# Kernel optimization log

Hardware: AMD Instinct MI355X
Metric: run time of the kernel (lower is better)

Reference implementation:

```python
import jax, jax.numpy as jnp
import numpy as np

GRID_SIZE = 5
SPLINE_ORDER = 3
GRID_RANGE = (-1.0, 1.0)
IN_FEATURES = 1024
OUT_FEATURES = 1024
N_TOKENS = 8192
N_BASIS = GRID_SIZE + SPLINE_ORDER  # number of B-spline basis functions per input feature


def make_grid(dtype=jnp.float32):
    # Extended knot vector: grid_size+1 interior knots over grid_range, padded by
    # spline_order knots on each side (efficient-KAN convention; the intended
    # semantics of the TF port's b_splines recursion).
    h = (GRID_RANGE[1] - GRID_RANGE[0]) / GRID_SIZE
    idx = jnp.arange(-SPLINE_ORDER, GRID_SIZE + SPLINE_ORDER + 1, dtype=dtype)
    return idx * h + GRID_RANGE[0]  # [grid_size + 2*spline_order + 1]


def b_splines(x, grid):
    # x: [N, in] -> bases: [N, in, N_BASIS] via de Boor / Cox recursion.
    x3 = x[..., None]  # [N, in, 1]
    g = grid  # [K], broadcasts against last axis
    bases = ((x3 >= g[:-1]) & (x3 < g[1:])).astype(x.dtype)  # order-0: [N, in, K-1]
    for k in range(1, SPLINE_ORDER + 1):
        left = (x3 - g[: -(k + 1)]) / (g[k:-1] - g[: -(k + 1)])
        right = (g[k + 1:] - x3) / (g[k + 1:] - g[1:-k])
        bases = left * bases[..., :-1] + right * bases[..., 1:]
    return bases  # [N, in, N_BASIS]


def setup_inputs() -> dict:
    key = jax.random.key(0)
    k1, k2, k3, k4 = jax.random.split(key, 4)
    x = jax.random.uniform(k1, (N_TOKENS, IN_FEATURES), dtype=jnp.float32)
    base_weight = jax.random.normal(k2, (IN_FEATURES, OUT_FEATURES), dtype=jnp.float32) * 0.02
    spline_weight = jax.random.normal(k3, (OUT_FEATURES, IN_FEATURES, N_BASIS), dtype=jnp.float32) * 0.02
    spline_scaler = jax.random.normal(k4, (OUT_FEATURES, IN_FEATURES), dtype=jnp.float32) * 0.1
    return {"x": x, "base_weight": base_weight, "spline_weight": spline_weight,
            "spline_scaler": spline_scaler}


def reference(x, base_weight, spline_weight, spline_scaler):
    grid = make_grid(x.dtype)
    # base path: silu(x) @ W_base
    base_out = jnp.matmul(jax.nn.silu(x), base_weight)  # [N, out]
    # spline path: grouped contraction over (in_feature, basis)
    bases = b_splines(x, grid)  # [N, in, nb]
    sw = spline_weight * spline_scaler[..., None]  # standalone scale: [out, in, nb]
    spline_out = jnp.einsum('nib,oib->no', bases, sw)
    return base_out + spline_out  # [N, out]
```

## Files before the change

kernel.cpp:

```cpp
#include <hip/hip_runtime.h>
#include <hip/hip_bf16.h>
#include <stdint.h>

typedef unsigned short u16;
typedef __attribute__((ext_vector_type(8))) __bf16 bf16x8;
typedef __attribute__((ext_vector_type(4))) float f32x4;

#define NTOK 8192
#define NIN  1024
#define NOUT 1024
#define KTOT 9216
#define BM 128
#define BN 256
#define BK 64
#define NT (KTOT / BK)
#define ABUF (BM * BK)
#define BBUF (BN * BK)
#define TBUF (ABUF + BBUF)

#define PB_BLOCKS 1024
#define PS_BLOCKS 4096
#define BA_BLOCKS 32768

__device__ __forceinline__ u16 f2bf(float f) {
  union { float f; unsigned u; } v; v.f = f;
  unsigned r = v.u + 0x7FFFu + ((v.u >> 16) & 1u);
  return (u16)(r >> 16);
}

__device__ __forceinline__ void gload_lds16(const void* g, void* l) {
  __builtin_amdgcn_global_load_lds(
      (__attribute__((address_space(1))) void*)(uintptr_t)g,
      (__attribute__((address_space(3))) void*)(uintptr_t)l, 16, 0, 0);
}

__global__ void prep_all(const float* __restrict__ X, const float* __restrict__ W,
                         const float* __restrict__ SW, const float* __restrict__ SS,
                         u16* __restrict__ Bt, u16* __restrict__ A) {
  __shared__ float tile[32][33];
  const int b = blockIdx.x;
  const int tid = threadIdx.x;

  if (b < PB_BLOCKS) {
    int i0 = (b & 31) * 32, o0 = (b >> 5) * 32;
    int tx = tid & 31, ty = tid >> 5;
#pragma unroll
    for (int r = 0; r < 4; ++r)
      tile[ty + 8 * r][tx] = W[(size_t)(i0 + ty + 8 * r) * NOUT + o0 + tx];
    __syncthreads();
#pragma unroll
    for (int r = 0; r < 4; ++r)
      Bt[(size_t)(o0 + ty + 8 * r) * KTOT + i0 + tx] = f2bf(tile[tx][ty + 8 * r]);
  } else if (b < PB_BLOCKS + PS_BLOCKS) {
    int idx = (b - PB_BLOCKS) * 256 + tid;
    int o = idx >> 10, i = idx & 1023;
    float s = SS[idx];
    const float4* p = (const float4*)(SW + (size_t)idx * 8);
    float4 a = p[0], c = p[1];
    union { u16 us[8]; uint4 v; } pk;
    pk.us[0] = f2bf(a.x * s); pk.us[1] = f2bf(a.y * s);
    pk.us[2] = f2bf(a.z * s); pk.us[3] = f2bf(a.w * s);
    pk.us[4] = f2bf(c.x * s); pk.us[5] = f2bf(c.y * s);
    pk.us[6] = f2bf(c.z * s); pk.us[7] = f2bf(c.w * s);
    *(uint4*)(Bt + (size_t)o * KTOT + NIN + (size_t)i * 8) = pk.v;
  } else {
    int idx = (b - PB_BLOCKS - PS_BLOCKS) * 256 + tid;
    int n = idx >> 10, i = idx & 1023;
    float x = X[idx];
    float sx = x / (1.f + __expf(-x));
    A[(size_t)n * KTOT + i] = f2bf(sx);
    float bb[11];
#pragma unroll
    for (int j = 0; j < 11; ++j) {
      float gj  = 0.4f * j - 2.2f;
      float gj1 = 0.4f * (j + 1) - 2.2f;
      bb[j] = (x >= gj && x < gj1) ? 1.f : 0.f;
    }
#pragma unroll
    for (int k = 1; k <= 3; ++k) {
      float inv = 1.f / (0.4f * k);
#pragma unroll
      for (int j = 0; j + k < 11; ++j) {
        float gj = 0.4f * j - 2.2f;
        float left  = (x - gj) * inv;
        float right = (0.4f * (j + k + 1) - 2.2f - x) * inv;
        bb[j] = left * bb[j] + right * bb[j + 1];
      }
    }
    union { u16 us[8]; uint4 v; } pk;
#pragma unroll
    for (int j = 0; j < 8; ++j) pk.us[j] = f2bf(bb[j]);
    *(uint4*)(A + (size_t)n * KTOT + NIN + (size_t)i * 8) = pk.v;
  }
}


__global__ __launch_bounds__(512, 2) void kan_gemm(const u16* __restrict__ A,
                                                   const u16* __restrict__ Bt,
                                                   float* __restrict__ C) {
  __shared__ u16 lds[3 * TBUF];
  const int tid = threadIdx.x;
  const int w = tid >> 6, l = tid & 63;
  const int wr = w >> 2, wc = w & 3;
  const int l4 = l >> 4, lc = l & 15;

  const int bid = blockIdx.x;
  const int xcd = bid & 7, jj = bid >> 3;
  const int bn = xcd >> 1;
  const int bm = (xcd & 1) * 32 + jj;

  const u16* Ab = A  + (size_t)bm * BM * KTOT;
  const u16* Bb = Bt + (size_t)bn * BN * KTOT;

  int srcA[2], dstA[2], srcB[4], dstB[4];
#pragma unroll
  for (int it = 0; it < 2; ++it) {
    int c = it * 512 + tid, r = c >> 3, s = (c & 7) ^ (r & 7);
    srcA[it] = r * KTOT + s * 8;
    dstA[it] = (it * 512 + w * 64) * 8;
  }
#pragma unroll
  for (int it = 0; it < 4; ++it) {
    int c = it * 512 + tid, r = c >> 3, s = (c & 7) ^ (r & 7);
    srcB[it] = r * KTOT + s * 8;
    dstB[it] = ABUF + (it * 512 + w * 64) * 8;
  }

  int rA[4], rB[4];
#pragma unroll
  for (int m = 0; m < 4; ++m) rA[m] = wr * 64 + m * 16 + lc;
#pragma unroll
  for (int n = 0; n < 4; ++n) rB[n] = wc * 64 + n * 16 + lc;

  f32x4 acc[4][4];
#pragma unroll
  for (int m = 0; m < 4; ++m)
#pragma unroll
    for (int n = 0; n < 4; ++n)
      acc[m][n] = f32x4{0.f, 0.f, 0.f, 0.f};

#pragma unroll
  for (int it = 0; it < 2; ++it) gload_lds16(Ab + srcA[it], &lds[dstA[it]]);
#pragma unroll
  for (int it = 0; it < 4; ++it) gload_lds16(Bb + srcB[it], &lds[dstB[it]]);
#pragma unroll
  for (int it = 0; it < 2; ++it) gload_lds16(Ab + srcA[it] + BK, &lds[TBUF + dstA[it]]);
#pragma unroll
  for (int it = 0; it < 4; ++it) gload_lds16(Bb + srcB[it] + BK, &lds[TBUF + dstB[it]]);
  asm volatile("s_waitcnt vmcnt(6)" ::: "memory");
  __builtin_amdgcn_s_barrier();

  int cur = 0;
  for (int t = 0; t < NT; ++t) {
    const int curo = cur * TBUF;
    const int nxto = ((cur == 0) ? 2 : cur - 1) * TBUF;
    const bool pf = (t + 2) < NT;
    const int k0n = (t + 2) * BK;

    if (pf) {
#pragma unroll
      for (int it = 0; it < 2; ++it) gload_lds16(Ab + srcA[it] + k0n, &lds[nxto + dstA[it]]);
#pragma unroll
      for (int it = 0; it < 4; ++it) gload_lds16(Bb + srcB[it] + k0n, &lds[nxto + dstB[it]]);
    }

    bf16x8 a_frag[4][2], b_frag[4][2];
#pragma unroll
    for (int m = 0; m < 4; ++m)
#pragma unroll
      for (int kk = 0; kk < 2; ++kk)
        a_frag[m][kk] = *(const bf16x8*)&lds[curo + rA[m] * 64 + (((kk * 4 + l4) ^ (rA[m] & 7)) * 8)];
#pragma unroll
    for (int n = 0; n < 4; ++n)
#pragma unroll
      for (int kk = 0; kk < 2; ++kk)
        b_frag[n][kk] = *(const bf16x8*)&lds[curo + ABUF + rB[n] * 64 + (((kk * 4 + l4) ^ (rB[n] & 7)) * 8)];

    asm volatile("s_waitcnt lgkmcnt(0)" ::: "memory");
    __builtin_amdgcn_sched_barrier(0);
    __builtin_amdgcn_s_setprio(1);
#pragma unroll
    for (int kk = 0; kk < 2; ++kk)
#pragma unroll
      for (int m = 0; m < 4; ++m)
#pragma unroll
        for (int n = 0; n < 4; ++n)
          acc[m][n] = __builtin_amdgcn_mfma_f32_16x16x32_bf16(a_frag[m][kk], b_frag[n][kk], acc[m][n], 0, 0, 0);
    __builtin_amdgcn_s_setprio(0);

    if (t >= NT - 2) { asm volatile("s_waitcnt vmcnt(0)" ::: "memory"); }
    else             { asm volatile("s_waitcnt vmcnt(6)" ::: "memory"); }
    __builtin_amdgcn_s_barrier();

    cur = (cur == 2) ? 0 : cur + 1;
  }

  const int row0 = bm * BM + wr * 64 + l4 * 4;
  const int col0 = bn * BN + wc * 64 + lc;
#pragma unroll
  for (int m = 0; m < 4; ++m)
#pragma unroll
    for (int n = 0; n < 4; ++n) {
      float* cp = C + (size_t)(row0 + m * 16) * NOUT + col0 + n * 16;
#pragma unroll
      for (int r = 0; r < 4; ++r)
        cp[(size_t)r * NOUT] = acc[m][n][r];
    }
}

extern "C" void kernel_launch(void* const* d_in, const int* in_sizes, int n_in,
                              void* d_out, int out_size, void* d_ws, size_t ws_size,
                              hipStream_t stream) {
  const float* x  = (const float*)d_in[0];
  const float* bw = (const float*)d_in[1];
  const float* sw = (const float*)d_in[2];
  const float* ss = (const float*)d_in[3];
  float* out = (float*)d_out;

  u16* Bt = (u16*)d_ws;
  u16* A  = (u16*)((char*)d_ws + (size_t)NOUT * KTOT * 2);

  prep_all<<<PB_BLOCKS + PS_BLOCKS + BA_BLOCKS, 256, 0, stream>>>(x, bw, sw, ss, Bt, A);
  kan_gemm<<<256, 512, 0, stream>>>(A, Bt, out);
}
```

Measured before the change: 281.3 us.

## Load A fragments directly from global into registers, bypassing LDS

The A operand is now fetched by each wave straight from global memory into registers, double-buffered one K-step ahead, and is no longer staged through LDS. Only the B tile goes through the triple-buffered LDS pipeline, which shrinks shared memory and removes the A LDS writes and reads. Waves that share rows of A now fetch the same data redundantly from global/L2. The vmcnt waits are retuned for the mixed register and LDS loads, and the loop is manually unrolled by two to alternate the A register buffers.

```diff
diff --git a/kernel.cpp b/kernel.cpp
--- a/kernel.cpp
+++ b/kernel.cpp
@@ -14,9 +14,7 @@
 #define BN 256
 #define BK 64
 #define NT (KTOT / BK)
-#define ABUF (BM * BK)
 #define BBUF (BN * BK)
-#define TBUF (ABUF + BBUF)
 
 #define PB_BLOCKS 1024
 #define PS_BLOCKS 4096
@@ -98,7 +96,7 @@
 __global__ __launch_bounds__(512, 2) void kan_gemm(const u16* __restrict__ A,
                                                    const u16* __restrict__ Bt,
                                                    float* __restrict__ C) {
-  __shared__ u16 lds[3 * TBUF];
+  __shared__ u16 lds[3 * BBUF];
   const int tid = threadIdx.x;
   const int w = tid >> 6, l = tid & 63;
   const int wr = w >> 2, wc = w & 3;
@@ -109,26 +107,19 @@
   const int bn = xcd >> 1;
   const int bm = (xcd & 1) * 32 + jj;
 
-  const u16* Ab = A  + (size_t)bm * BM * KTOT;
   const u16* Bb = Bt + (size_t)bn * BN * KTOT;
-
-  int srcA[2], dstA[2], srcB[4], dstB[4];
-#pragma unroll
-  for (int it = 0; it < 2; ++it) {
-    int c = it * 512 + tid, r = c >> 3, s = (c & 7) ^ (r & 7);
-    srcA[it] = r * KTOT + s * 8;
-    dstA[it] = (it * 512 + w * 64) * 8;
-  }
+  const u16* aBase = A + (size_t)(bm * 128 + wr * 64 + lc) * KTOT + l4 * 8;
+#define MSTRIDE ((size_t)16 * KTOT)
+
+  int srcB[4], dstB[4];
 #pragma unroll
   for (int it = 0; it < 4; ++it) {
     int c = it * 512 + tid, r = c >> 3, s = (c & 7) ^ (r & 7);
     srcB[it] = r * KTOT + s * 8;
-    dstB[it] = ABUF + (it * 512 + w * 64) * 8;
+    dstB[it] = (it * 512 + w * 64) * 8;
   }
 
-  int rA[4], rB[4];
-#pragma unroll
-  for (int m = 0; m < 4; ++m) rA[m] = wr * 64 + m * 16 + lc;
+  int rB[4];
 #pragma unroll
   for (int n = 0; n < 4; ++n) rB[n] = wc * 64 + n * 16 + lc;
 
@@ -139,60 +130,103 @@
     for (int n = 0; n < 4; ++n)
       acc[m][n] = f32x4{0.f, 0.f, 0.f, 0.f};
 
-#pragma unroll
-  for (int it = 0; it < 2; ++it) gload_lds16(Ab + srcA[it], &lds[dstA[it]]);
+  bf16x8 pA0[4][2], pA1[4][2];
+
+#pragma unroll
+  for (int m = 0; m < 4; ++m)
+#pragma unroll
+    for (int kk = 0; kk < 2; ++kk)
+      pA0[m][kk] = *(const bf16x8*)(aBase + m * MSTRIDE + kk * 32);
 #pragma unroll
   for (int it = 0; it < 4; ++it) gload_lds16(Bb + srcB[it], &lds[dstB[it]]);
 #pragma unroll
-  for (int it = 0; it < 2; ++it) gload_lds16(Ab + srcA[it] + BK, &lds[TBUF + dstA[it]]);
-#pragma unroll
-  for (int it = 0; it < 4; ++it) gload_lds16(Bb + srcB[it] + BK, &lds[TBUF + dstB[it]]);
-  asm volatile("s_waitcnt vmcnt(6)" ::: "memory");
+  for (int it = 0; it < 4; ++it) gload_lds16(Bb + srcB[it] + BK, &lds[BBUF + dstB[it]]);
+  asm volatile("s_waitcnt vmcnt(4)" ::: "memory");
   __builtin_amdgcn_s_barrier();
 
   int cur = 0;
-  for (int t = 0; t < NT; ++t) {
-    const int curo = cur * TBUF;
-    const int nxto = ((cur == 0) ? 2 : cur - 1) * TBUF;
-    const bool pf = (t + 2) < NT;
-    const int k0n = (t + 2) * BK;
-
-    if (pf) {
-#pragma unroll
-      for (int it = 0; it < 2; ++it) gload_lds16(Ab + srcA[it] + k0n, &lds[nxto + dstA[it]]);
-#pragma unroll
-      for (int it = 0; it < 4; ++it) gload_lds16(Bb + srcB[it] + k0n, &lds[nxto + dstB[it]]);
-    }
-
-    bf16x8 a_frag[4][2], b_frag[4][2];
-#pragma unroll
-    for (int m = 0; m < 4; ++m)
+#pragma unroll 1
+  for (int tp = 0; tp < NT / 2; ++tp) {
+    {
+      const int t = 2 * tp;
+      const int curo = cur * BBUF;
+      const int nxto = ((cur == 0) ? 2 : cur - 1) * BBUF;
+      const u16* aT1 = aBase + (size_t)(t + 1) * BK;
+
+#pragma unroll
+      for (int m = 0; m < 4; ++m)
+#pragma unroll
+        for (int kk = 0; kk < 2; ++kk)
+          pA1[m][kk] = *(const bf16x8*)(aT1 + m * MSTRIDE + kk * 32);
+      if (t + 2 < NT) {
+        const int k0n = (t + 2) * BK;
+#pragma unroll
+        for (int it = 0; it < 4; ++it) gload_lds16(Bb + srcB[it] + k0n, &lds[nxto + dstB[it]]);
+      }
+      __builtin_amdgcn_sched_barrier(0);
+      bf16x8 b_frag[4][2];
+#pragma unroll
+      for (int n = 0; n < 4; ++n)
+#pragma unroll
+        for (int kk = 0; kk < 2; ++kk)
+          b_frag[n][kk] = *(const bf16x8*)&lds[curo + rB[n] * 64 + (((kk * 4 + l4) ^ (rB[n] & 7)) * 8)];
+      asm volatile("s_waitcnt lgkmcnt(0)" ::: "memory");
+      __builtin_amdgcn_sched_barrier(0);
+      __builtin_amdgcn_s_setprio(1);
 #pragma unroll
       for (int kk = 0; kk < 2; ++kk)
-        a_frag[m][kk] = *(const bf16x8*)&lds[curo + rA[m] * 64 + (((kk * 4 + l4) ^ (rA[m] & 7)) * 8)];
-#pragma unroll
-    for (int n = 0; n < 4; ++n)
+#pragma unroll
+        for (int m = 0; m < 4; ++m)
+#pragma unroll
+          for (int n = 0; n < 4; ++n)
+            acc[m][n] = __builtin_amdgcn_mfma_f32_16x16x32_bf16(pA0[m][kk], b_frag[n][kk], acc[m][n], 0, 0, 0);
+      __builtin_amdgcn_s_setprio(0);
+      if (t == NT - 2) { asm volatile("s_waitcnt vmcnt(8)" ::: "memory"); }
+      else             { asm volatile("s_waitcnt vmcnt(12)" ::: "memory"); }
+      __builtin_amdgcn_s_barrier();
+      cur = (cur == 2) ? 0 : cur + 1;
+    }
+    {
+      const int t = 2 * tp + 1;
+      const int curo = cur * BBUF;
+      const int nxto = ((cur == 0) ? 2 : cur - 1) * BBUF;
+      const u16* aT1 = aBase + (size_t)(t + 1) * BK;
+
+      if (t + 1 < NT) {
+#pragma unroll
+        for (int m = 0; m < 4; ++m)
+#pragma unroll
+          for (int kk = 0; kk < 2; ++kk)
+            pA0[m][kk] = *(const bf16x8*)(aT1 + m * MSTRIDE + kk * 32);
+      }
+      if (t + 2 < NT) {
+        const int k0n = (t + 2) * BK;
+#pragma unroll
+        for (int it = 0; it < 4; ++it) gload_lds16(Bb + srcB[it] + k0n, &lds[nxto + dstB[it]]);
+      }
+      __builtin_amdgcn_sched_barrier(0);
+      bf16x8 b_frag[4][2];
+#pragma unroll
+      for (int n = 0; n < 4; ++n)
+#pragma unroll
+        for (int kk = 0; kk < 2; ++kk)
+          b_frag[n][kk] = *(const bf16x8*)&lds[curo + rB[n] * 64 + (((kk * 4 + l4) ^ (rB[n] & 7)) * 8)];
+      asm volatile("s_waitcnt lgkmcnt(0)" ::: "memory");
+      __builtin_amdgcn_sched_barrier(0);
+      __builtin_amdgcn_s_setprio(1);
 #pragma unroll
       for (int kk = 0; kk < 2; ++kk)
-        b_frag[n][kk] = *(const bf16x8*)&lds[curo + ABUF + rB[n] * 64 + (((kk * 4 + l4) ^ (rB[n] & 7)) * 8)];
-
-    asm volatile("s_waitcnt lgkmcnt(0)" ::: "memory");
-    __builtin_amdgcn_sched_barrier(0);
-    __builtin_amdgcn_s_setprio(1);
-#pragma unroll
-    for (int kk = 0; kk < 2; ++kk)
-#pragma unroll
-      for (int m = 0; m < 4; ++m)
-#pragma unroll
-        for (int n = 0; n < 4; ++n)
-          acc[m][n] = __builtin_amdgcn_mfma_f32_16x16x32_bf16(a_frag[m][kk], b_frag[n][kk], acc[m][n], 0, 0, 0);
-    __builtin_amdgcn_s_setprio(0);
-
-    if (t >= NT - 2) { asm volatile("s_waitcnt vmcnt(0)" ::: "memory"); }
-    else             { asm volatile("s_waitcnt vmcnt(6)" ::: "memory"); }
-    __builtin_amdgcn_s_barrier();
-
-    cur = (cur == 2) ? 0 : cur + 1;
+#pragma unroll
+        for (int m = 0; m < 4; ++m)
+#pragma unroll
+          for (int n = 0; n < 4; ++n)
+            acc[m][n] = __builtin_amdgcn_mfma_f32_16x16x32_bf16(pA1[m][kk], b_frag[n][kk], acc[m][n], 0, 0, 0);
+      __builtin_amdgcn_s_setprio(0);
+      if (t == NT - 1)      { asm volatile("s_waitcnt vmcnt(0)"  ::: "memory"); }
+      else                  { asm volatile("s_waitcnt vmcnt(12)" ::: "memory"); }
+      __builtin_amdgcn_s_barrier();
+      cur = (cur == 2) ? 0 : cur + 1;
+    }
   }
 
   const int row0 = bm * BM + wr * 64 + l4 * 4;
```

New measurement: 486.8 us. 73.1% more time.
